# Optimization experiments

Hardware: AMD Instinct MI355X
Metric: run time of the kernel (lower is better)

The kernel has to match this reference:

```python
import jax, jax.numpy as jnp
import numpy as np

EPS = 1e-8  # torch CosineSimilarity eps


def _cosine_sim_matrix(x, y):
    # x: [Nx, D], y: [Ny, D] -> [Nx, Ny] cosine similarity via normalized GEMM
    xn = x / jnp.maximum(jnp.linalg.norm(x, axis=-1, keepdims=True), EPS)
    yn = y / jnp.maximum(jnp.linalg.norm(y, axis=-1, keepdims=True), EPS)
    return xn @ yn.T


def setup_inputs() -> dict:
    key = jax.random.key(0)
    k1, k2, k3, k4 = jax.random.split(key, 4)
    N, D, C = 4096, 512, 100
    inst_embed = jax.random.normal(k1, (N, D), dtype=jnp.float32)
    proxy = jax.random.normal(k2, (N, D), dtype=jnp.float32)
    # binary positive-selection mask per class over the batch
    negative_mask = (jax.random.uniform(k3, (C, N)) > 0.5).astype(jnp.float32)
    labels = jax.random.randint(k4, (N,), 0, C, dtype=jnp.int64)
    temperature = jnp.float32(0.1)
    margin = jnp.float32(0.0)
    return {"inst_embed": inst_embed, "proxy": proxy,
            "negative_mask": negative_mask, "labels": labels,
            "temperature": temperature, "margin": margin}


def reference(inst_embed, proxy, negative_mask, labels, temperature, margin):
    # [N, N] similarity matrices
    p2i = _cosine_sim_matrix(proxy, inst_embed)
    i2i = _cosine_sim_matrix(inst_embed, inst_embed)
    p2i_zone = jnp.exp((p2i - margin) / temperature)
    i2i_zone = jnp.exp((i2i - margin) / temperature)
    mask = negative_mask[labels]  # [N, N]
    p2i_num = (p2i_zone * mask).sum(axis=1)
    i2i_num = (i2i_zone * mask).sum(axis=1)
    p2i_den = p2i_zone.sum(axis=1)
    i2i_den = i2i_zone.sum(axis=1)
    p2i_loss = -jnp.log(temperature * (p2i_num / p2i_den)).mean()
    i2i_loss = -jnp.log(temperature * (i2i_num / i2i_den)).mean()
    return p2i_loss + i2i_loss
```

## Files before the change

### kernel.cpp

```cpp
#include <hip/hip_runtime.h>
#include <hip/hip_bf16.h>

#define D_DIM 512
#define KSTEPS 16
#define BM 64
#define BN 32
#define GRIDY 8

typedef __bf16 bf16x8 __attribute__((ext_vector_type(8)));
typedef float  f32x4  __attribute__((ext_vector_type(4)));

__device__ __forceinline__ unsigned short f2bf_rne(float x) {
    unsigned int u = __float_as_uint(x);
    u += 0x7FFFu + ((u >> 16) & 1u);
    return (unsigned short)(u >> 16);
}

__device__ __forceinline__ void g2l16(const void* g, void* l) {
    __builtin_amdgcn_global_load_lds(
        (const __attribute__((address_space(1))) unsigned int*)g,
        (__attribute__((address_space(3))) unsigned int*)l, 16, 0, 0);
}

__global__ __launch_bounds__(256) void normalize_rows(
    const float* __restrict__ inst, const float* __restrict__ proxy,
    unsigned short* __restrict__ instb, unsigned short* __restrict__ proxyb,
    float* __restrict__ nd, int N)
{
    const int lane = threadIdx.x & 63;
    const int wave = threadIdx.x >> 6;
    const int base = blockIdx.x * 16 + wave * 4;
    #pragma unroll
    for (int i = 0; i < 4; ++i) {
        const int row = base + i;
        const float* src;
        unsigned short* dst;
        if (row < N) { src = inst  + (size_t)row * D_DIM;        dst = instb  + (size_t)row * D_DIM; }
        else         { src = proxy + (size_t)(row - N) * D_DIM;  dst = proxyb + (size_t)(row - N) * D_DIM; }
        float4 v0 = ((const float4*)src)[lane * 2];
        float4 v1 = ((const float4*)src)[lane * 2 + 1];
        float ss = v0.x*v0.x + v0.y*v0.y + v0.z*v0.z + v0.w*v0.w
                 + v1.x*v1.x + v1.y*v1.y + v1.z*v1.z + v1.w*v1.w;
        #pragma unroll
        for (int off = 32; off > 0; off >>= 1) ss += __shfl_xor(ss, off, 64);
        const float inv = 1.0f / fmaxf(sqrtf(ss), 1e-8f);
        ushort4 o0, o1;
        o0.x = f2bf_rne(v0.x * inv); o0.y = f2bf_rne(v0.y * inv);
        o0.z = f2bf_rne(v0.z * inv); o0.w = f2bf_rne(v0.w * inv);
        o1.x = f2bf_rne(v1.x * inv); o1.y = f2bf_rne(v1.y * inv);
        o1.z = f2bf_rne(v1.z * inv); o1.w = f2bf_rne(v1.w * inv);
        ((ushort4*)dst)[lane * 2]     = o0;
        ((ushort4*)dst)[lane * 2 + 1] = o1;
    }
    if (blockIdx.x < 16)
        ((float4*)nd)[blockIdx.x * 256 + threadIdx.x] = make_float4(0.f, 0.f, 0.f, 0.f);
}

__global__ __launch_bounds__(256) __attribute__((amdgpu_waves_per_eu(2, 2)))
void fused_scores(
    const unsigned short* __restrict__ instb,
    const unsigned short* __restrict__ proxyb,
    const float* __restrict__ negmask,
    const int*  __restrict__ labels,
    const float* __restrict__ temp_p,
    const float* __restrict__ margin_p,
    float* __restrict__ nd,
    int N, int colsPerBlock)
{
    __shared__ unsigned short Bt0[BN * D_DIM];
    __shared__ unsigned short Bt1[BN * D_DIM];

    const int tid  = threadIdx.x;
    const int lane = tid & 63;
    const int wave = tid >> 6;
    const int quad = lane >> 4;
    const int l16  = lane & 15;

    const int row0 = blockIdx.x * BM + wave * 16;

    const float temp  = *temp_p;
    const float scale = 1.44269504088896340736f / temp;
    const float bias  = -(*margin_p) * scale;

    bf16x8 Ap[KSTEPS], Ai[KSTEPS];
    {
        const unsigned short* pr = proxyb + (size_t)(row0 + l16) * D_DIM + quad * 8;
        const unsigned short* ir = instb  + (size_t)(row0 + l16) * D_DIM + quad * 8;
        #pragma unroll
        for (int ks = 0; ks < KSTEPS; ks++) {
            Ap[ks] = *(const bf16x8*)(pr + ks * 32);
            Ai[ks] = *(const bf16x8*)(ir + ks * 32);
        }
        #pragma unroll
        for (int ks = 0; ks < KSTEPS; ks++)
            asm volatile("" : "+v"(Ap[ks]), "+v"(Ai[ks]));
    }

    int lab[4];
    #pragma unroll
    for (int r = 0; r < 4; r++) lab[r] = labels[row0 + quad * 4 + r];

    float numP[4] = {0.f,0.f,0.f,0.f}, denP[4] = {0.f,0.f,0.f,0.f};
    float numI[4] = {0.f,0.f,0.f,0.f}, denI[4] = {0.f,0.f,0.f,0.f};

    const int j0base = blockIdx.y * colsPerBlock;
    const int nt     = colsPerBlock / BN;

    auto stage = [&](unsigned short (&B)[BN * D_DIM], int t) {
        const int j0 = j0base + t * BN;
        #pragma unroll
        for (int it = 0; it < BN / 4; ++it) {
            const int br = it * 4 + wave;
            const unsigned short* src =
                instb + (size_t)(j0 + br) * D_DIM + ((lane ^ (br & 7)) * 8);
            g2l16(src, &B[br * D_DIM]);
        }
    };

    auto compute = [&](unsigned short (&B)[BN * D_DIM], int t) {
        const int j0 = j0base + t * BN;
        float mk0[4], mk1[4];
        #pragma unroll
        for (int r = 0; r < 4; ++r) {
            mk0[r] = negmask[(size_t)lab[r] * N + (j0 + l16)];
            mk1[r] = negmask[(size_t)lab[r] * N + (j0 + 16 + l16)];
        }
        f32x4 accP[2] = {}, accI[2] = {};
        #pragma unroll
        for (int ks = 0; ks < KSTEPS; ++ks) {
            #pragma unroll
            for (int cg = 0; cg < 2; ++cg) {
                const int rB  = cg * 16 + l16;
                const int chs = (ks * 4 + quad) ^ (rB & 7);
                bf16x8 b = *(const bf16x8*)&B[(size_t)rB * D_DIM + chs * 8];
                accP[cg] = __builtin_amdgcn_mfma_f32_16x16x32_bf16(Ap[ks], b, accP[cg], 0, 0, 0);
                accI[cg] = __builtin_amdgcn_mfma_f32_16x16x32_bf16(Ai[ks], b, accI[cg], 0, 0, 0);
            }
        }
        #pragma unroll
        for (int r = 0; r < 4; ++r) {
            float zp0 = exp2f(accP[0][r] * scale + bias);
            float zi0 = exp2f(accI[0][r] * scale + bias);
            float zp1 = exp2f(accP[1][r] * scale + bias);
            float zi1 = exp2f(accI[1][r] * scale + bias);
            denP[r] += zp0 + zp1; numP[r] += zp0 * mk0[r] + zp1 * mk1[r];
            denI[r] += zi0 + zi1; numI[r] += zi0 * mk0[r] + zi1 * mk1[r];
        }
    };

    stage(Bt0, 0);
    __syncthreads();
    for (int t = 0; t < nt; t += 2) {
        stage(Bt1, t + 1);
        compute(Bt0, t);
        __syncthreads();
        if (t + 2 < nt) stage(Bt0, t + 2);
        compute(Bt1, t + 1);
        __syncthreads();
    }

    #pragma unroll
    for (int r = 0; r < 4; r++) {
        float np = numP[r], dp = denP[r], ni = numI[r], di = denI[r];
        #pragma unroll
        for (int off = 8; off > 0; off >>= 1) {
            np += __shfl_down(np, off, 16);
            dp += __shfl_down(dp, off, 16);
            ni += __shfl_down(ni, off, 16);
            di += __shfl_down(di, off, 16);
        }
        if (l16 == 0) {
            const int row = row0 + quad * 4 + r;
            atomicAdd(&nd[row],         np);
            atomicAdd(&nd[N + row],     dp);
            atomicAdd(&nd[2 * N + row], ni);
            atomicAdd(&nd[3 * N + row], di);
        }
    }
}

__global__ __launch_bounds__(1024) void loss_reduce(
    const float* __restrict__ nd, const float* __restrict__ temp_p,
    float* __restrict__ out, int N)
{
    const float t = *temp_p;
    float s = 0.f;
    for (int i = threadIdx.x; i < N; i += 1024) {
        s += (logf(nd[N + i])     - logf(nd[i]));
        s += (logf(nd[3 * N + i]) - logf(nd[2 * N + i]));
    }
    #pragma unroll
    for (int off = 32; off > 0; off >>= 1) s += __shfl_down(s, off, 64);
    __shared__ float wss[16];
    if ((threadIdx.x & 63) == 0) wss[threadIdx.x >> 6] = s;
    __syncthreads();
    if (threadIdx.x < 16) {
        float v = wss[threadIdx.x];
        #pragma unroll
        for (int off = 8; off > 0; off >>= 1) v += __shfl_down(v, off, 16);
        if (threadIdx.x == 0) out[0] = v / (float)N - 2.0f * logf(t);
    }
}

extern "C" void kernel_launch(void* const* d_in, const int* in_sizes, int n_in,
                              void* d_out, int out_size, void* d_ws, size_t ws_size,
                              hipStream_t stream)
{
    const float* inst     = (const float*)d_in[0];
    const float* proxy    = (const float*)d_in[1];
    const float* negmask  = (const float*)d_in[2];
    const int*   labels   = (const int*)d_in[3];
    const float* temp_p   = (const float*)d_in[4];
    const float* margin_p = (const float*)d_in[5];
    float* out = (float*)d_out;

    const int N = in_sizes[3];

    unsigned short* instb  = (unsigned short*)d_ws;
    unsigned short* proxyb = instb + (size_t)N * D_DIM;
    float* nd = (float*)(proxyb + (size_t)N * D_DIM);

    normalize_rows<<<2 * N / 16, 256, 0, stream>>>(inst, proxy, instb, proxyb, nd, N);
    dim3 grid(N / BM, GRIDY);
    fused_scores<<<grid, 256, 0, stream>>>(instb, proxyb, negmask, labels,
                                           temp_p, margin_p, nd, N, N / GRIDY);
    loss_reduce<<<1, 1024, 0, stream>>>(nd, temp_p, out, N);
}
```

Baseline: 124.7 us.

## Interleave B-tile prefetch with phased MFMA groups using explicit LDS reads

Each 32-column tile's compute is split into four phases. Each phase issues eight explicit ds_read_b128 loads, waits for them, then runs sixteen MFMAs at raised wave priority. The global-to-LDS staging of the next tile is spread in quarters between the phases, synchronised by raw s_barrier and vmcnt waits instead of full __syncthreads, so memory traffic and LDS reads overlap with matrix math. The 2D grid is flattened so the eight column-blocks of a row tile run adjacently, and the register-pinning asm on the A fragments is removed. The last tile now prefetches one tile past its column range unconditionally, and the hand-written wait counts make correctness depend on exact instruction ordering.

```diff
diff --git a/kernel.cpp b/kernel.cpp
--- a/kernel.cpp
+++ b/kernel.cpp
@@ -20,6 +20,47 @@
     __builtin_amdgcn_global_load_lds(
         (const __attribute__((address_space(1))) unsigned int*)g,
         (__attribute__((address_space(3))) unsigned int*)l, 16, 0, 0);
+}
+
+__device__ __forceinline__ unsigned lds_addr(const void* p) {
+    return (unsigned)(uintptr_t)(const __attribute__((address_space(3))) void*)p;
+}
+
+template <int P>
+__device__ __forceinline__ void phase_mfma(
+    const unsigned (&ad)[2][2],
+    const bf16x8 (&Ap)[KSTEPS], const bf16x8 (&Ai)[KSTEPS],
+    f32x4 (&aP)[2], f32x4 (&aI)[2])
+{
+    bf16x8 b00, b01, b10, b11, b20, b21, b30, b31;
+    asm volatile("ds_read_b128 %0, %1 offset:%2" : "=v"(b00) : "v"(ad[0][0]), "i"(P * 256));
+    asm volatile("ds_read_b128 %0, %1 offset:%2" : "=v"(b01) : "v"(ad[1][0]), "i"(P * 256));
+    asm volatile("ds_read_b128 %0, %1 offset:%2" : "=v"(b10) : "v"(ad[0][1]), "i"(P * 256));
+    asm volatile("ds_read_b128 %0, %1 offset:%2" : "=v"(b11) : "v"(ad[1][1]), "i"(P * 256));
+    asm volatile("ds_read_b128 %0, %1 offset:%2" : "=v"(b20) : "v"(ad[0][0]), "i"(P * 256 + 128));
+    asm volatile("ds_read_b128 %0, %1 offset:%2" : "=v"(b21) : "v"(ad[1][0]), "i"(P * 256 + 128));
+    asm volatile("ds_read_b128 %0, %1 offset:%2" : "=v"(b30) : "v"(ad[0][1]), "i"(P * 256 + 128));
+    asm volatile("ds_read_b128 %0, %1 offset:%2" : "=v"(b31) : "v"(ad[1][1]), "i"(P * 256 + 128));
+    asm volatile("s_waitcnt lgkmcnt(0)" ::: "memory");
+    __builtin_amdgcn_sched_barrier(0);
+    __builtin_amdgcn_s_setprio(1);
+    aP[0] = __builtin_amdgcn_mfma_f32_16x16x32_bf16(Ap[P*4+0], b00, aP[0], 0, 0, 0);
+    aI[0] = __builtin_amdgcn_mfma_f32_16x16x32_bf16(Ai[P*4+0], b00, aI[0], 0, 0, 0);
+    aP[1] = __builtin_amdgcn_mfma_f32_16x16x32_bf16(Ap[P*4+0], b01, aP[1], 0, 0, 0);
+    aI[1] = __builtin_amdgcn_mfma_f32_16x16x32_bf16(Ai[P*4+0], b01, aI[1], 0, 0, 0);
+    aP[0] = __builtin_amdgcn_mfma_f32_16x16x32_bf16(Ap[P*4+1], b10, aP[0], 0, 0, 0);
+    aI[0] = __builtin_amdgcn_mfma_f32_16x16x32_bf16(Ai[P*4+1], b10, aI[0], 0, 0, 0);
+    aP[1] = __builtin_amdgcn_mfma_f32_16x16x32_bf16(Ap[P*4+1], b11, aP[1], 0, 0, 0);
+    aI[1] = __builtin_amdgcn_mfma_f32_16x16x32_bf16(Ai[P*4+1], b11, aI[1], 0, 0, 0);
+    aP[0] = __builtin_amdgcn_mfma_f32_16x16x32_bf16(Ap[P*4+2], b20, aP[0], 0, 0, 0);
+    aI[0] = __builtin_amdgcn_mfma_f32_16x16x32_bf16(Ai[P*4+2], b20, aI[0], 0, 0, 0);
+    aP[1] = __builtin_amdgcn_mfma_f32_16x16x32_bf16(Ap[P*4+2], b21, aP[1], 0, 0, 0);
+    aI[1] = __builtin_amdgcn_mfma_f32_16x16x32_bf16(Ai[P*4+2], b21, aI[1], 0, 0, 0);
+    aP[0] = __builtin_amdgcn_mfma_f32_16x16x32_bf16(Ap[P*4+3], b30, aP[0], 0, 0, 0);
+    aI[0] = __builtin_amdgcn_mfma_f32_16x16x32_bf16(Ai[P*4+3], b30, aI[0], 0, 0, 0);
+    aP[1] = __builtin_amdgcn_mfma_f32_16x16x32_bf16(Ap[P*4+3], b31, aP[1], 0, 0, 0);
+    aI[1] = __builtin_amdgcn_mfma_f32_16x16x32_bf16(Ai[P*4+3], b31, aI[1], 0, 0, 0);
+    __builtin_amdgcn_s_setprio(0);
 }
 
 __global__ __launch_bounds__(256) void normalize_rows(
@@ -56,8 +97,7 @@
         ((float4*)nd)[blockIdx.x * 256 + threadIdx.x] = make_float4(0.f, 0.f, 0.f, 0.f);
 }
 
-__global__ __launch_bounds__(256) __attribute__((amdgpu_waves_per_eu(2, 2)))
-void fused_scores(
+__global__ __launch_bounds__(256, 2) void fused_scores(
     const unsigned short* __restrict__ instb,
     const unsigned short* __restrict__ proxyb,
     const float* __restrict__ negmask,
@@ -76,7 +116,11 @@
     const int quad = lane >> 4;
     const int l16  = lane & 15;
 
-    const int row0 = blockIdx.x * BM + wave * 16;
+    const int bx = blockIdx.x >> 3;
+    const int by = blockIdx.x & 7;
+
+    const int row0   = bx * BM + wave * 16;
+    const int j0base = by * colsPerBlock;
 
     const float temp  = *temp_p;
     const float scale = 1.44269504088896340736f / temp;
@@ -91,9 +135,6 @@
             Ap[ks] = *(const bf16x8*)(pr + ks * 32);
             Ai[ks] = *(const bf16x8*)(ir + ks * 32);
         }
-        #pragma unroll
-        for (int ks = 0; ks < KSTEPS; ks++)
-            asm volatile("" : "+v"(Ap[ks]), "+v"(Ai[ks]));
     }
 
     int lab[4];
@@ -103,60 +144,78 @@
     float numP[4] = {0.f,0.f,0.f,0.f}, denP[4] = {0.f,0.f,0.f,0.f};
     float numI[4] = {0.f,0.f,0.f,0.f}, denI[4] = {0.f,0.f,0.f,0.f};
 
-    const int j0base = blockIdx.y * colsPerBlock;
-    const int nt     = colsPerBlock / BN;
-
-    auto stage = [&](unsigned short (&B)[BN * D_DIM], int t) {
-        const int j0 = j0base + t * BN;
-        #pragma unroll
-        for (int it = 0; it < BN / 4; ++it) {
+    const int r3 = l16 & 7;
+    unsigned off_[2][2];
+    #pragma unroll
+    for (int cg = 0; cg < 2; ++cg)
+        #pragma unroll
+        for (int e = 0; e < 2; ++e)
+            off_[cg][e] = (unsigned)((cg * 16 + l16) * (D_DIM * 2)
+                        + ((((e << 2) ^ (r3 & 4)) | (quad ^ (r3 & 3))) * 16));
+
+    const int nt = colsPerBlock / BN;
+
+    auto stage_pair = [&](unsigned short* B, int jsrc, int q) {
+        #pragma unroll
+        for (int s = 0; s < 2; ++s) {
+            const int it = q * 2 + s;
             const int br = it * 4 + wave;
             const unsigned short* src =
-                instb + (size_t)(j0 + br) * D_DIM + ((lane ^ (br & 7)) * 8);
-            g2l16(src, &B[br * D_DIM]);
+                instb + (size_t)(jsrc + br) * D_DIM + ((lane ^ (br & 7)) * 8);
+            g2l16(src, B + (size_t)br * D_DIM);
         }
     };
 
-    auto compute = [&](unsigned short (&B)[BN * D_DIM], int t) {
-        const int j0 = j0base + t * BN;
+    auto do_tile = [&](const unsigned short* curB, unsigned short* nxtB, int j0) {
+        unsigned ad[2][2];
+        const unsigned cb = lds_addr(curB);
+        #pragma unroll
+        for (int cg = 0; cg < 2; ++cg)
+            #pragma unroll
+            for (int e = 0; e < 2; ++e) ad[cg][e] = cb + off_[cg][e];
+
+        stage_pair(nxtB, j0 + BN, 0);
+        asm volatile("s_waitcnt vmcnt(2)" ::: "memory");
+        __builtin_amdgcn_s_barrier();
+
         float mk0[4], mk1[4];
         #pragma unroll
         for (int r = 0; r < 4; ++r) {
             mk0[r] = negmask[(size_t)lab[r] * N + (j0 + l16)];
             mk1[r] = negmask[(size_t)lab[r] * N + (j0 + 16 + l16)];
         }
-        f32x4 accP[2] = {}, accI[2] = {};
-        #pragma unroll
-        for (int ks = 0; ks < KSTEPS; ++ks) {
-            #pragma unroll
-            for (int cg = 0; cg < 2; ++cg) {
-                const int rB  = cg * 16 + l16;
-                const int chs = (ks * 4 + quad) ^ (rB & 7);
-                bf16x8 b = *(const bf16x8*)&B[(size_t)rB * D_DIM + chs * 8];
-                accP[cg] = __builtin_amdgcn_mfma_f32_16x16x32_bf16(Ap[ks], b, accP[cg], 0, 0, 0);
-                accI[cg] = __builtin_amdgcn_mfma_f32_16x16x32_bf16(Ai[ks], b, accI[cg], 0, 0, 0);
-            }
-        }
+
+        f32x4 aP[2] = {}, aI[2] = {};
+        phase_mfma<0>(ad, Ap, Ai, aP, aI);
+        stage_pair(nxtB, j0 + BN, 1);
+        __builtin_amdgcn_s_barrier();
+        phase_mfma<1>(ad, Ap, Ai, aP, aI);
+        stage_pair(nxtB, j0 + BN, 2);
+        __builtin_amdgcn_s_barrier();
+        phase_mfma<2>(ad, Ap, Ai, aP, aI);
+        stage_pair(nxtB, j0 + BN, 3);
+        __builtin_amdgcn_s_barrier();
+        phase_mfma<3>(ad, Ap, Ai, aP, aI);
+
         #pragma unroll
         for (int r = 0; r < 4; ++r) {
-            float zp0 = exp2f(accP[0][r] * scale + bias);
-            float zi0 = exp2f(accI[0][r] * scale + bias);
-            float zp1 = exp2f(accP[1][r] * scale + bias);
-            float zi1 = exp2f(accI[1][r] * scale + bias);
+            float zp0 = exp2f(aP[0][r] * scale + bias);
+            float zi0 = exp2f(aI[0][r] * scale + bias);
+            float zp1 = exp2f(aP[1][r] * scale + bias);
+            float zi1 = exp2f(aI[1][r] * scale + bias);
             denP[r] += zp0 + zp1; numP[r] += zp0 * mk0[r] + zp1 * mk1[r];
             denI[r] += zi0 + zi1; numI[r] += zi0 * mk0[r] + zi1 * mk1[r];
         }
+
+        __builtin_amdgcn_s_barrier();
     };
 
-    stage(Bt0, 0);
-    __syncthreads();
+    #pragma unroll
+    for (int q = 0; q < 4; ++q) stage_pair(Bt0, j0base, q);
+
     for (int t = 0; t < nt; t += 2) {
-        stage(Bt1, t + 1);
-        compute(Bt0, t);
-        __syncthreads();
-        if (t + 2 < nt) stage(Bt0, t + 2);
-        compute(Bt1, t + 1);
-        __syncthreads();
+        do_tile(Bt0, Bt1, j0base + t * BN);
+        do_tile(Bt1, Bt0, j0base + (t + 1) * BN);
     }
 
     #pragma unroll
@@ -221,8 +280,7 @@
     float* nd = (float*)(proxyb + (size_t)N * D_DIM);
 
     normalize_rows<<<2 * N / 16, 256, 0, stream>>>(inst, proxy, instb, proxyb, nd, N);
-    dim3 grid(N / BM, GRIDY);
-    fused_scores<<<grid, 256, 0, stream>>>(instb, proxyb, negmask, labels,
-                                           temp_p, margin_p, nd, N, N / GRIDY);
+    fused_scores<<<(N / BM) * GRIDY, 256, 0, stream>>>(instb, proxyb, negmask, labels,
+                                                       temp_p, margin_p, nd, N, N / GRIDY);
     loss_reduce<<<1, 1024, 0, stream>>>(nd, temp_p, out, N);
 }
```

After: 149.8 us. 20.1% more time.
